# Kernel tuning notes

Hardware: AMD Instinct MI355X
Metric: run time of the kernel (lower is better)

The kernel has to match this reference:

```python
import jax, jax.numpy as jnp
import numpy as np

B, C, H, W = 32, 256, 32, 32


def setup_inputs() -> dict:
    key = jax.random.key(0)
    k1, k2, k3 = jax.random.split(key, 3)
    h = jax.random.normal(k1, (B, C, H, W), dtype=jnp.float32)
    w1_w = jax.random.normal(k2, (1, C), dtype=jnp.float32) * (1.0 / np.sqrt(C))
    w1_b = jnp.zeros((1,), dtype=jnp.float32)
    w2_w = jax.random.normal(k3, (1, C), dtype=jnp.float32) * (1.0 / np.sqrt(C))
    w2_b = jnp.zeros((1,), dtype=jnp.float32)
    return {"h": h, "w1_w": w1_w, "w1_b": w1_b, "w2_w": w2_w, "w2_b": w2_b}


def reference(h, w1_w, w1_b, w2_w, w2_b):
    b, c, hh, ww = h.shape
    x = jnp.transpose(h, (0, 2, 3, 1))            # [B,H,W,C]
    # scalar projections of every spatial token
    a = jnp.einsum('bhwc,c->bhw', x, w1_w[0]) + w1_b[0]   # query-side scalar [B,H,W]
    k = jnp.einsum('bhwc,c->bhw', x, w2_w[0]) + w2_b[0]   # key-side scalar   [B,H,W]
    n = hh * ww
    # additive attention scores over all spatial pairs: [B,H,W,HW]
    scores = jnp.tanh(a[:, :, :, None] + k.reshape(b, 1, 1, n))
    attn = jax.nn.softmax(scores, axis=-1)                 # exp(tanh)/sum == softmax(tanh)
    ctx = jnp.einsum('bijn,bnc->bijc', attn, x.reshape(b, n, c))  # [B,H,W,C]
    out = jnp.where(ctx >= 0, ctx, 0.2 * ctx)              # LeakyReLU(0.2)
    return jnp.transpose(out, (0, 3, 1, 2))                # [B,C,H,W]
```

## Files before the change

kernel.cpp:

```cpp
#include <hip/hip_runtime.h>

constexpr int Bn = 32;
constexpr int Cn = 256;
constexpr int Nn = 1024;

constexpr float C2 = 2.8853900817779268f;
constexpr float K1 = 1.4426950408889634f;

typedef __bf16 v8bf  __attribute__((ext_vector_type(8)));
typedef float  v16f  __attribute__((ext_vector_type(16)));


__device__ __forceinline__ void async16(const void* g, void* l) {
    __builtin_amdgcn_global_load_lds(
        (const __attribute__((address_space(1))) unsigned int*)g,
        (__attribute__((address_space(3))) unsigned int*)l, 16, 0, 0);
}

__global__ __launch_bounds__(256) void prep_kernel(
    const float* __restrict__ h,
    const float* __restrict__ w1, const float* __restrict__ w1b,
    const float* __restrict__ w2, const float* __restrict__ w2b,
    float* __restrict__ pa_g, float* __restrict__ q_g,
    unsigned char* __restrict__ hbf)
{
    int blk = blockIdx.x;
    int xcd = blk & 7, idx = blk >> 3;
    int b   = xcd * 4 + (idx >> 4);
    int n0  = (idx & 15) * 64;
    int t = threadIdx.x, cq = t >> 6, l = t & 63;

    const float* hb = h + (size_t)b * Cn * Nn + n0 + l;
    int nt32 = (n0 >> 5) + (l >> 5);
    unsigned char* wb = hbf + ((size_t)(b * 32 + nt32)) * 16384 + ((l & 7) << 1);
    int g = (l >> 3) & 3;

    float s1 = 0.f, s2 = 0.f;
#pragma unroll 8
    for (int ci = 0; ci < 64; ++ci) {
        int c = cq * 64 + ci;
        float v = hb[(size_t)c * Nn];
        s1 = fmaf(v, w1[c], s1);
        s2 = fmaf(v, w2[c], s2);
        union { __bf16 bv; unsigned short us; } u;
        u.bv = (__bf16)v;
        *(unsigned short*)(wb + c * 64 + ((g ^ (c & 3)) << 4)) = u.us;
    }
    __shared__ float p1[4][64], p2[4][64];
    p1[cq][l] = s1;
    p2[cq][l] = s2;
    __syncthreads();
    if (t < 64) {
        float a = p1[0][t] + p1[1][t] + p1[2][t] + p1[3][t] + w1b[0];
        float k = p2[0][t] + p2[1][t] + p2[2][t] + p2[3][t] + w2b[0];
        pa_g[b * Nn + n0 + t] = exp2f(C2 * a);
        q_g [b * Nn + n0 + t] = exp2f(C2 * k);
    }
}

constexpr int EST_OFF  = 32768;
constexpr int QS_OFF   = 65792;
constexpr int SP_OFF   = 69888;
constexpr int SINV_OFF = 71936;
constexpr int CTX_SMEM = 72192;

__global__ __launch_bounds__(512, 4) void ctx_kernel(
    const unsigned char* __restrict__ hbf,
    const float* __restrict__ pa_g, const float* __restrict__ q_g,
    float* __restrict__ out)
{
    __shared__ alignas(16) unsigned char smem[CTX_SMEM];
    float* qs           = (float*)(smem + QS_OFF);
    float (*Sp)[64]     = (float(*)[64])(smem + SP_OFF);
    float* Sinv         = (float*)(smem + SINV_OFF);
    float (*comb)[257]  = (float(*)[257])smem;

    int blk = blockIdx.x;
    int xcd = blk & 7, slot = blk >> 3;
    int b   = xcd * 4 + (slot >> 4);
    int i0  = (slot & 15) * 64;

    int t = threadIdx.x, w = t >> 6, l = t & 63;
    int lm = l & 31, lh = l >> 5;
    int cq = w & 3, wq = w >> 2;

    const unsigned char* hbf_b = hbf + (size_t)b * 524288;

    for (int i = t; i < Nn; i += 512) qs[i] = q_g[b * Nn + i];
    float pav = pa_g[b * Nn + i0 + l];

    v16f acc[2][2];
#pragma unroll
    for (int x = 0; x < 2; ++x)
#pragma unroll
        for (int y = 0; y < 2; ++y)
#pragma unroll
            for (int r = 0; r < 16; ++r) acc[x][y][r] = 0.f;
    float Spart = 0.f;

    unsigned char* estw = smem + EST_OFF + l * 128 + ((w ^ (l & 7)) << 4);

    for (int tt = 0; tt < 16; ++tt) {
        __syncthreads();
#pragma unroll
        for (int p = 0; p < 4; ++p) {
            int id = p * 8 + w;
            int hh = id >> 4, off = (id & 15) << 10;
            const unsigned char* src = hbf_b + (((hh << 4) + tt) << 14) + off + (l << 4);
            async16(src, smem + (hh << 14) + off);
        }
        {
            int qb = (w >> 2) * 512 + tt * 32 + (w & 3) * 8;
            float4 q0 = *(const float4*)&qs[qb];
            float4 q1 = *(const float4*)&qs[qb + 4];
            float qv[8] = {q0.x, q0.y, q0.z, q0.w, q1.x, q1.y, q1.z, q1.w};
            v8bf ev;
#pragma unroll
            for (int j = 0; j < 8; ++j) {
                float z = pav * qv[j];
                float r = __builtin_amdgcn_rcpf(1.f + z);
                float e = exp2f(fmaf(r, -2.f * K1, K1));
                __bf16 eb = (__bf16)e;
                ev[j] = eb;
                Spart += (float)eb;
            }
            *(v8bf*)estw = ev;
        }
        __syncthreads();
#pragma unroll
        for (int ks = 0; ks < 2; ++ks) {
            int gA = ((wq << 2) + (ks << 1) + lh) ^ (lm & 7);
            v8bf a0 = *(const v8bf*)(smem + EST_OFF + lm * 128        + (gA << 4));
            v8bf a1 = *(const v8bf*)(smem + EST_OFF + (32 + lm) * 128 + (gA << 4));
            int gB = ((ks << 1) + lh) ^ (lm & 3);
            const unsigned char* bB = smem + (wq << 14) + (cq * 64 + lm) * 64;
            v8bf b0 = *(const v8bf*)(bB +        (gB << 4));
            v8bf b1 = *(const v8bf*)(bB + 2048 + (gB << 4));
            acc[0][0] = __builtin_amdgcn_mfma_f32_32x32x16_bf16(a0, b0, acc[0][0], 0, 0, 0);
            acc[0][1] = __builtin_amdgcn_mfma_f32_32x32x16_bf16(a0, b1, acc[0][1], 0, 0, 0);
            acc[1][0] = __builtin_amdgcn_mfma_f32_32x32x16_bf16(a1, b0, acc[1][0], 0, 0, 0);
            acc[1][1] = __builtin_amdgcn_mfma_f32_32x32x16_bf16(a1, b1, acc[1][1], 0, 0, 0);
        }
    }

    Sp[w][l] = Spart;
    __syncthreads();
    if (t < 64) {
        float S = 0.f;
#pragma unroll
        for (int ww = 0; ww < 8; ++ww) S += Sp[ww][t];
        Sinv[t] = 1.f / S;
    }
    if (wq == 1) {
#pragma unroll
        for (int x = 0; x < 2; ++x)
#pragma unroll
            for (int y = 0; y < 2; ++y)
#pragma unroll
                for (int r = 0; r < 16; ++r) {
                    int rl = (r & 3) + 8 * (r >> 2) + 4 * lh;
                    comb[x * 32 + rl][cq * 64 + y * 32 + lm] = acc[x][y][r];
                }
    }
    __syncthreads();
    if (wq == 0) {
#pragma unroll
        for (int x = 0; x < 2; ++x)
#pragma unroll
            for (int y = 0; y < 2; ++y)
#pragma unroll
                for (int r = 0; r < 16; ++r) {
                    int rl  = (r & 3) + 8 * (r >> 2) + 4 * lh;
                    int row = x * 32 + rl;
                    int col = cq * 64 + y * 32 + lm;
                    float v = (acc[x][y][r] + comb[row][col]) * Sinv[row];
                    v = (v >= 0.f) ? v : 0.2f * v;
                    comb[row][col] = v;
                }
    }
    __syncthreads();
    float* ob = out + (size_t)b * Cn * Nn + i0;
#pragma unroll
    for (int p = 0; p < 8; ++p) {
        int slot = t + (p << 9);
        int c    = slot >> 4;
        int i4   = (slot & 15) << 2;
        float4 o;
        o.x = comb[i4 + 0][c];
        o.y = comb[i4 + 1][c];
        o.z = comb[i4 + 2][c];
        o.w = comb[i4 + 3][c];
        *(float4*)(ob + (size_t)c * Nn + i4) = o;
    }
}

extern "C" void kernel_launch(void* const* d_in, const int* in_sizes, int n_in,
                              void* d_out, int out_size, void* d_ws, size_t ws_size,
                              hipStream_t stream) {
    const float* h   = (const float*)d_in[0];
    const float* w1w = (const float*)d_in[1];
    const float* w1b = (const float*)d_in[2];
    const float* w2w = (const float*)d_in[3];
    const float* w2b = (const float*)d_in[4];
    float* out = (float*)d_out;

    float* pa_ws = (float*)d_ws;
    float* q_ws  = pa_ws + Bn * Nn;
    unsigned char* hbf = (unsigned char*)d_ws + 262144;

    prep_kernel<<<512, 256, 0, stream>>>(h, w1w, w1b, w2w, w2b, pa_ws, q_ws, hbf);
    ctx_kernel <<<512, 512, 0, stream>>>(hbf, pa_ws, q_ws, out);
}
```

Measured before the change: 123.1 us.

## Stage prep tile through LDS to write packed 16-byte bf16 chunks

The prep kernel now stages each 64-channel chunk of h through a shared-memory tile and transposes it. Each thread packs eight bf16 values and writes them as one 16-byte store into the swizzled hbf layout, replacing scattered 2-byte global stores. This is meant to cut the write-transaction overhead of building the bf16 copy, at the cost of extra LDS traffic and barriers. The ctx_kernel launch bound also drops from a minimum of 4 to 2 waves per EU, which relaxes the register limit and may lower occupancy.

```diff
diff --git a/kernel.cpp b/kernel.cpp
--- a/kernel.cpp
+++ b/kernel.cpp
@@ -28,27 +28,48 @@
     int xcd = blk & 7, idx = blk >> 3;
     int b   = xcd * 4 + (idx >> 4);
     int n0  = (idx & 15) * 64;
-    int t = threadIdx.x, cq = t >> 6, l = t & 63;
-
-    const float* hb = h + (size_t)b * Cn * Nn + n0 + l;
-    int nt32 = (n0 >> 5) + (l >> 5);
-    unsigned char* wb = hbf + ((size_t)(b * 32 + nt32)) * 16384 + ((l & 7) << 1);
-    int g = (l >> 3) & 3;
-
+    int t = threadIdx.x, w = t >> 6, l = t & 63;
+
+    __shared__ float lds_t[64][68];
+    __shared__ float p1[4][64], p2[4][64];
+
+    const float* hb = h + (size_t)b * Cn * Nn + n0;
     float s1 = 0.f, s2 = 0.f;
-#pragma unroll 8
-    for (int ci = 0; ci < 64; ++ci) {
-        int c = cq * 64 + ci;
-        float v = hb[(size_t)c * Nn];
-        s1 = fmaf(v, w1[c], s1);
-        s2 = fmaf(v, w2[c], s2);
-        union { __bf16 bv; unsigned short us; } u;
-        u.bv = (__bf16)v;
-        *(unsigned short*)(wb + c * 64 + ((g ^ (c & 3)) << 4)) = u.us;
-    }
-    __shared__ float p1[4][64], p2[4][64];
-    p1[cq][l] = s1;
-    p2[cq][l] = s2;
+
+    int nt32  = (n0 >> 5) + (w >> 1);
+    int gbase = (w & 1) * 2;
+    unsigned char* nt_base = hbf + (size_t)(b * 32 + nt32) * 16384;
+
+    for (int chunk = 0; chunk < 4; ++chunk) {
+        if (chunk) __syncthreads();
+#pragma unroll 4
+        for (int ci = 0; ci < 16; ++ci) {
+            int c = chunk * 64 + w * 16 + ci;
+            float v = hb[(size_t)c * Nn + l];
+            s1 = fmaf(v, w1[c], s1);
+            s2 = fmaf(v, w2[c], s2);
+            lds_t[w * 16 + ci][l] = v;
+        }
+        __syncthreads();
+        int c = chunk * 64 + l;
+        unsigned char* crow = nt_base + c * 64;
+#pragma unroll
+        for (int g2 = 0; g2 < 2; ++g2) {
+            int g = gbase + g2;
+            int col = (w >> 1) * 32 + g * 8;
+            float4 va = *(const float4*)&lds_t[l][col];
+            float4 vb = *(const float4*)&lds_t[l][col + 4];
+            union { __bf16 bx[8]; uint4 u4; } pk;
+            pk.bx[0] = (__bf16)va.x; pk.bx[1] = (__bf16)va.y;
+            pk.bx[2] = (__bf16)va.z; pk.bx[3] = (__bf16)va.w;
+            pk.bx[4] = (__bf16)vb.x; pk.bx[5] = (__bf16)vb.y;
+            pk.bx[6] = (__bf16)vb.z; pk.bx[7] = (__bf16)vb.w;
+            *(uint4*)(crow + ((g ^ (c & 3)) << 4)) = pk.u4;
+        }
+    }
+
+    p1[w][l] = s1;
+    p2[w][l] = s2;
     __syncthreads();
     if (t < 64) {
         float a = p1[0][t] + p1[1][t] + p1[2][t] + p1[3][t] + w1b[0];
@@ -64,7 +85,7 @@
 constexpr int SINV_OFF = 71936;
 constexpr int CTX_SMEM = 72192;
 
-__global__ __launch_bounds__(512, 4) void ctx_kernel(
+__global__ __launch_bounds__(512, 2) void ctx_kernel(
     const unsigned char* __restrict__ hbf,
     const float* __restrict__ pa_g, const float* __restrict__ q_g,
     float* __restrict__ out)
```

Result: slower. 128.4 us (+4.3%).
